# Kernel optimization log

Measured on AMD Instinct MI355X. Metric: run time of the kernel, lower is better.

The kernel has to match this reference:

```python
import jax, jax.numpy as jnp
import numpy as np

B, S, E = 4, 2048, 1024
H, D, F = 16, 64, 4096
EPS = 1e-5


def layer_norm(x, gamma, beta):
    mu = jnp.mean(x, axis=-1, keepdims=True)
    var = jnp.mean(jnp.square(x - mu), axis=-1, keepdims=True)
    return (x - mu) * jax.lax.rsqrt(var + EPS) * gamma + beta


def setup_inputs() -> dict:
    key = jax.random.key(0)
    ks = jax.random.split(key, 8)
    scale = 0.02  # keep logits in a numerically sane range
    X = jax.random.normal(ks[0], (B, S, E), dtype=jnp.float32)
    WQ = jax.random.normal(ks[1], (H, E, D), dtype=jnp.float32) * scale
    WK = jax.random.normal(ks[2], (H, E, D), dtype=jnp.float32) * scale
    WV = jax.random.normal(ks[3], (H, E, D), dtype=jnp.float32) * scale
    WO = jax.random.normal(ks[4], (H * D, E), dtype=jnp.float32) * scale
    gamma = jnp.ones((E,), dtype=jnp.float32)
    beta = jnp.zeros((E,), dtype=jnp.float32)
    W1 = jax.random.normal(ks[5], (E, F), dtype=jnp.float32) * scale
    b1 = jnp.zeros((F,), dtype=jnp.float32)
    W2 = jax.random.normal(ks[6], (F, E), dtype=jnp.float32) * scale
    b2 = jnp.zeros((E,), dtype=jnp.float32)
    return {"X": X, "WQ": WQ, "WK": WK, "WV": WV, "WO": WO,
            "gamma": gamma, "beta": beta, "W1": W1, "b1": b1, "W2": W2, "b2": b2}


def reference(X, WQ, WK, WV, WO, gamma, beta, W1, b1, W2, b2):
    # Batched-over-heads version of the per-head python loop (same math).
    Q = jnp.einsum('bse,hed->bhsd', X, WQ)  # [B,H,S,D]
    K = jnp.einsum('bse,hed->bhsd', X, WK)
    V = jnp.einsum('bse,hed->bhsd', X, WV)
    scores = jnp.einsum('bhsd,bhtd->bhst', Q, K)  # [B,H,S,T]
    # FAITHFUL quirk: torch.softmax(..., dim=1) on a [B,S,S] tensor normalizes
    # over the QUERY axis (axis=2 here), then divides by sqrt(D) AFTER softmax.
    att = jax.nn.softmax(scores, axis=2) / jnp.sqrt(jnp.float32(D))
    vec = jnp.einsum('bhst,bhtd->bhsd', att, V)  # [B,H,S,D]
    att_vec = jnp.transpose(vec, (0, 2, 1, 3)).reshape(X.shape[0], X.shape[1], H * D)
    vector_att = layer_norm(att_vec @ WO + X, gamma, beta)
    vector_ffn = jax.nn.relu(vector_att @ W1 + b1) @ W2 + b2
    return layer_norm(vector_ffn + vector_att, gamma, beta)
```

## Files before the change

kernel.cpp:

```cpp
#include <hip/hip_runtime.h>
#include <cstddef>
#include <cstdint>

#define BB 4
#define SS 2048
#define EE 1024
#define HH 16
#define DD 64
#define FF 4096

typedef unsigned short u16;
typedef __attribute__((ext_vector_type(8))) short short8;
typedef __attribute__((ext_vector_type(4))) short short4v;
typedef __attribute__((ext_vector_type(4))) float f32x4;
typedef __attribute__((ext_vector_type(16))) float f32x16;
typedef __attribute__((ext_vector_type(4))) unsigned u32x4;

__device__ __forceinline__ u16 f2bf(float x) {
    unsigned u = __builtin_bit_cast(unsigned, x);
    u += 0x7fffu + ((u >> 16) & 1u);
    return (u16)(u >> 16);
}
__device__ __forceinline__ float bf2f(u16 h) {
    unsigned u = ((unsigned)h) << 16;
    return __builtin_bit_cast(float, u);
}
__device__ __forceinline__ float ex2(float x) {
    float r;
    asm("v_exp_f32 %0, %1" : "=v"(r) : "v"(x));
    return r;
}
__device__ __forceinline__ unsigned cvtpk(float lo, float hi) {
    unsigned r;
    asm("v_cvt_pk_bf16_f32 %0, %1, %2" : "=v"(r) : "v"(lo), "v"(hi));
    return r;
}
__device__ __forceinline__ void pl32swap(unsigned &a, unsigned &b) {
    asm("s_nop 1\n\tv_permlane32_swap_b32 %0, %1\n\ts_nop 1" : "+v"(a), "+v"(b));
}
__device__ __forceinline__ int sw(int row, int lbyte) {
    return row * 128 + (lbyte ^ ((row & 7) << 4));
}

#define GLD_LDS16(g, l)                                                     \
    __builtin_amdgcn_global_load_lds(                                       \
        (const __attribute__((address_space(1))) void*)(g),                 \
        (__attribute__((address_space(3))) void*)(l), 16, 0, 0)

__global__ __launch_bounds__(256) void cvt_bf(const float* __restrict__ in,
                                              u16* __restrict__ out, int n4) {
    const int i = blockIdx.x * 256 + threadIdx.x;
    if (i < n4) {
        float4 v = reinterpret_cast<const float4*>(in)[i];
        short4v o;
        o.x = (short)f2bf(v.x); o.y = (short)f2bf(v.y);
        o.z = (short)f2bf(v.z); o.w = (short)f2bf(v.w);
        reinterpret_cast<short4v*>(out)[i] = o;
    }
}

__global__ __launch_bounds__(256) void transp_bf(const float* __restrict__ in,
                                                 u16* __restrict__ out, int R, int C) {
    __shared__ float T[64][65];
    const int r0 = blockIdx.x * 64, c0 = blockIdx.y * 64;
    const size_t zoff = (size_t)blockIdx.z * R * C;
    in += zoff; out += zoff;
    const int tid = threadIdx.x;
#pragma unroll 4
    for (int i = 0; i < 16; ++i) {
        int l = tid + i * 256;
        T[l >> 6][l & 63] = in[(size_t)(r0 + (l >> 6)) * C + c0 + (l & 63)];
    }
    __syncthreads();
#pragma unroll 4
    for (int i = 0; i < 16; ++i) {
        int l = tid + i * 256;
        out[(size_t)(c0 + (l >> 6)) * R + r0 + (l & 63)] = f2bf(T[l & 63][l >> 6]);
    }
}

#define WAITV6 asm volatile("s_waitcnt vmcnt(6)" ::: "memory")
#define WAITV0 asm volatile("s_waitcnt vmcnt(0)" ::: "memory")

#define STAGE(p, k0u)                                                         \
    do {                                                                      \
        _Pragma("unroll")                                                     \
        for (int i_ = 0; i_ < 4; ++i_)                                        \
            GLD_LDS16(Ag + (size_t)(i_ * 64) * K + (k0u),                     \
                      &lds[(p) * 24576 + (i_ * 64 + w * 8) * 64]);            \
        _Pragma("unroll")                                                     \
        for (int j_ = 0; j_ < 2; ++j_)                                        \
            GLD_LDS16(Bg + (size_t)(j_ * 64) * K + (k0u),                     \
                      &lds[(p) * 24576 + 16384 + (j_ * 64 + w * 8) * 64]);    \
    } while (0)

template <int EPI>
__global__ __launch_bounds__(512, 2) void gemm256(const u16* __restrict__ A,
                                                  const u16* __restrict__ BT,
                                                  int K, int N, int gy,
                                                  void* __restrict__ Cout,
                                                  const float* __restrict__ bias,
                                                  const void* __restrict__ resid,
                                                  float oscale) {
    __shared__ __align__(16) u16 lds[2 * 24576];
    const int nwg = gridDim.x;
    const int bid = blockIdx.x;
    const int qq = nwg >> 3, rr = nwg & 7;
    const int xcd = bid & 7, lin = bid >> 3;
    const int wgid = (xcd < rr ? xcd * (qq + 1) : rr * (qq + 1) + (xcd - rr) * qq) + lin;
    const int x = wgid / gy, y = wgid % gy;
    const int m0 = x * 256, n0 = y * 128;

    const int tid = threadIdx.x;
    const int w = tid >> 6, l = tid & 63;
    const int l32 = l & 31, hf = l >> 5;
    const int wm = w >> 1, wn = w & 1;

    const int swz = ((l & 7) ^ (l >> 3)) * 8;
    const u16* Ag = A + (size_t)(m0 + w * 8 + (l >> 3)) * K + swz;
    const u16* Bg = BT + (size_t)(n0 + w * 8 + (l >> 3)) * K + swz;

    const int NTt = K >> 6;
    f32x16 acc[2][2] = {};

    STAGE(0, 0);
    STAGE(1, 64);

    for (int t = 0; t < NTt; ++t) {
        const int p = t & 1;
        if (t < NTt - 1) { WAITV6; } else { WAITV0; }
        __builtin_amdgcn_sched_barrier(0);
        __builtin_amdgcn_s_barrier();
        __builtin_amdgcn_sched_barrier(0);
        __builtin_amdgcn_s_setprio(1);
        const u16* Ab = &lds[p * 24576];
        const u16* Bb = &lds[p * 24576 + 16384];
#pragma unroll
        for (int kt = 0; kt < 4; ++kt) {
            const int cs = (((kt * 2 + hf) ^ (l32 & 7)) * 8);
            short8 af[2], bfr[2];
#pragma unroll
            for (int mb = 0; mb < 2; ++mb)
                af[mb] = *(const short8*)&Ab[(wm * 64 + mb * 32 + l32) * 64 + cs];
#pragma unroll
            for (int nb = 0; nb < 2; ++nb)
                bfr[nb] = *(const short8*)&Bb[(wn * 64 + nb * 32 + l32) * 64 + cs];
#pragma unroll
            for (int mb = 0; mb < 2; ++mb)
#pragma unroll
                for (int nb = 0; nb < 2; ++nb)
                    acc[mb][nb] = __builtin_amdgcn_mfma_f32_32x32x16_bf16(af[mb], bfr[nb], acc[mb][nb], 0, 0, 0);
        }
        __builtin_amdgcn_s_setprio(0);
        __builtin_amdgcn_sched_barrier(0);
        __builtin_amdgcn_s_barrier();
        __builtin_amdgcn_sched_barrier(0);
        if (t + 2 < NTt) STAGE(p, (t + 2) * 64);
    }

#pragma unroll
    for (int mb = 0; mb < 2; ++mb)
#pragma unroll
        for (int nb = 0; nb < 2; ++nb) {
            const int col = n0 + wn * 64 + nb * 32 + l32;
#pragma unroll
            for (int r = 0; r < 16; ++r) {
                const int row = m0 + wm * 64 + mb * 32 + (r & 3) + 8 * (r >> 2) + 4 * hf;
                float v = acc[mb][nb][r];
                const size_t idx = (size_t)row * N + col;
                if (EPI == 0) {
                    ((u16*)Cout)[idx] = f2bf(v * oscale);
                } else if (EPI == 1) {
                    ((float*)Cout)[idx] = v + ((const float*)resid)[idx];
                } else if (EPI == 2) {
                    v += bias[col];
                    ((u16*)Cout)[idx] = f2bf(fmaxf(v, 0.f));
                } else {
                    v += bias[col] + bf2f(((const u16*)resid)[idx]);
                    ((float*)Cout)[idx] = v;
                }
            }
        }
}

__global__ __launch_bounds__(256) void stats_l(const u16* __restrict__ Qg,
                                               const u16* __restrict__ Kg,
                                               float* __restrict__ Ls) {
    __shared__ u16 Qt[64 * 72];
    const int t0 = blockIdx.x * 128;
    const int bh = blockIdx.y;
    const int b = bh >> 4, h = bh & 15;
    const int tid = threadIdx.x;
    const int w = tid >> 6, l = tid & 63;
    const int quad = l >> 4, lane16 = l & 15;
    const u16* Qp = Qg + (size_t)b * SS * 1024 + h * 64;
    const u16* Kp = Kg + (size_t)b * SS * 1024 + h * 64;
    const int sr = tid >> 3;
    const int dg = (tid & 7) * 8;

    short8 kf[2][2];
#pragma unroll
    for (int nf = 0; nf < 2; ++nf)
#pragma unroll
        for (int ks = 0; ks < 2; ++ks)
            kf[nf][ks] = *(const short8*)(Kp +
                (size_t)(t0 + w * 32 + nf * 16 + lane16) * 1024 + ks * 32 + quad * 8);

    const u16* qsrc0 = Qp + (size_t)sr * 1024 + dg;
    short8 pq0 = *(const short8*)qsrc0;
    short8 pq1 = *(const short8*)(qsrc0 + (size_t)32 * 1024);

    float lcol[2] = {0.f, 0.f};
    for (int st = 0; st < 32; ++st) {
        __syncthreads();
        *(short8*)&Qt[sr * 72 + dg] = pq0;
        *(short8*)&Qt[(sr + 32) * 72 + dg] = pq1;
        __syncthreads();
        if (st + 1 < 32) {
            const u16* qsrc = Qp + (size_t)((st + 1) * 64 + sr) * 1024 + dg;
            pq0 = *(const short8*)qsrc;
            pq1 = *(const short8*)(qsrc + (size_t)32 * 1024);
        }
        f32x4 sc[4][2] = {};
#pragma unroll
        for (int ks = 0; ks < 2; ++ks) {
#pragma unroll
            for (int mf = 0; mf < 4; ++mf) {
                short8 afr = *(const short8*)&Qt[(mf * 16 + lane16) * 72 + ks * 32 + quad * 8];
#pragma unroll
                for (int nf = 0; nf < 2; ++nf)
                    sc[mf][nf] = __builtin_amdgcn_mfma_f32_16x16x32_bf16(afr, kf[nf][ks], sc[mf][nf], 0, 0, 0);
            }
        }
#pragma unroll
        for (int nf = 0; nf < 2; ++nf)
#pragma unroll
            for (int mf = 0; mf < 4; ++mf)
#pragma unroll
                for (int r = 0; r < 4; ++r) lcol[nf] += ex2(sc[mf][nf][r]);
    }
#pragma unroll
    for (int nf = 0; nf < 2; ++nf) {
        lcol[nf] += __shfl_xor(lcol[nf], 32);
        lcol[nf] += __shfl_xor(lcol[nf], 16);
        if (quad == 0)
            Ls[(size_t)bh * SS + t0 + w * 32 + nf * 16 + lane16] = lcol[nf];
    }
}

__global__ __launch_bounds__(256) void vscale(u16* __restrict__ Vtg,
                                              const float* __restrict__ Ls) {
    const int r = blockIdx.x;
    const int b = blockIdx.y;
    const int h = r >> 6;
    const int t0 = threadIdx.x * 8;
    u16* vp = Vtg + (size_t)r * 8192 + b * SS + t0;
    const float* lp = Ls + (size_t)(b * 16 + h) * SS + t0;
    short8 v = *(short8*)vp;
    short8 o;
#pragma unroll
    for (int i = 0; i < 8; ++i)
        o[i] = (short)f2bf(bf2f((u16)v[i]) * (0.125f / lp[i]));
    *(short8*)vp = o;
}

__global__ __launch_bounds__(256) void pv_fused(const u16* __restrict__ Qg,
                                                const u16* __restrict__ Kg,
                                                const u16* __restrict__ Vtg,
                                                u16* __restrict__ vecbf) {
    __shared__ u16 Ks[64 * 64];
    __shared__ u16 Vs[64 * 64];
    const int s0 = blockIdx.x * 128;
    const int bh = blockIdx.y;
    const int b = bh >> 4, h = bh & 15;
    const int tid = threadIdx.x;
    const int w = tid >> 6, l = tid & 63;
    const int l32 = l & 31, hf = l >> 5;
    const u16* Qp = Qg + (size_t)b * SS * 1024 + h * 64;
    const u16* Kp = Kg + (size_t)b * SS * 1024 + h * 64;
    const u16* Vp = Vtg + (size_t)h * 64 * 8192 + (size_t)b * SS;
    const int sr = tid >> 3, dg = (tid & 7) * 8;

    short8 qf[4];
#pragma unroll
    for (int ks = 0; ks < 4; ++ks)
        qf[ks] = *(const short8*)(Qp + (size_t)(s0 + w * 32 + l32) * 1024 + ks * 16 + hf * 8);

    short8 pk0 = *(const short8*)(Kp + (size_t)sr * 1024 + dg);
    short8 pk1 = *(const short8*)(Kp + (size_t)(sr + 32) * 1024 + dg);
    short8 pv0 = *(const short8*)(Vp + (size_t)sr * 8192 + dg);
    short8 pv1 = *(const short8*)(Vp + (size_t)(sr + 32) * 8192 + dg);

    f32x16 acc[2] = {};
    for (int tt = 0; tt < 32; ++tt) {
        __syncthreads();
        *(short8*)((char*)Ks + sw(sr, dg * 2)) = pk0;
        *(short8*)((char*)Ks + sw(sr + 32, dg * 2)) = pk1;
        *(short8*)((char*)Vs + sw(sr, dg * 2)) = pv0;
        *(short8*)((char*)Vs + sw(sr + 32, dg * 2)) = pv1;
        __syncthreads();
        if (tt + 1 < 32) {
            const int t1 = (tt + 1) * 64;
            pk0 = *(const short8*)(Kp + (size_t)(t1 + sr) * 1024 + dg);
            pk1 = *(const short8*)(Kp + (size_t)(t1 + sr + 32) * 1024 + dg);
            pv0 = *(const short8*)(Vp + (size_t)sr * 8192 + t1 + dg);
            pv1 = *(const short8*)(Vp + (size_t)(sr + 32) * 8192 + t1 + dg);
        }
        f32x16 sc0 = {}, sc1 = {};
#pragma unroll
        for (int ks = 0; ks < 4; ++ks) {
            short8 a0 = *(const short8*)((char*)Ks + sw(l32, ks * 32 + hf * 16));
            short8 a1 = *(const short8*)((char*)Ks + sw(32 + l32, ks * 32 + hf * 16));
            sc0 = __builtin_amdgcn_mfma_f32_32x32x16_bf16(a0, qf[ks], sc0, 0, 0, 0);
            sc1 = __builtin_amdgcn_mfma_f32_32x32x16_bf16(a1, qf[ks], sc1, 0, 0, 0);
        }
        unsigned cp0[8], cp1[8];
#pragma unroll
        for (int p = 0; p < 8; ++p) {
            cp0[p] = cvtpk(ex2(sc0[2 * p]), ex2(sc0[2 * p + 1]));
            cp1[p] = cvtpk(ex2(sc1[2 * p]), ex2(sc1[2 * p + 1]));
        }
        short8 pa[4];
#pragma unroll
        for (int ks2 = 0; ks2 < 4; ++ks2) {
            unsigned* cp = (ks2 & 2) ? cp1 : cp0;
            const int c = (ks2 & 1) * 4;
            unsigned w0 = cp[c + 0], w2 = cp[c + 2];
            unsigned w1 = cp[c + 1], w3 = cp[c + 3];
            pl32swap(w0, w2);
            pl32swap(w1, w3);
            u32x4 t4; t4.x = w0; t4.y = w1; t4.z = w2; t4.w = w3;
            pa[ks2] = __builtin_bit_cast(short8, t4);
        }
#pragma unroll
        for (int ks2 = 0; ks2 < 4; ++ks2)
#pragma unroll
            for (int nf = 0; nf < 2; ++nf) {
                short8 bfr = *(const short8*)((char*)Vs + sw(nf * 32 + l32, ks2 * 32 + hf * 16));
                acc[nf] = __builtin_amdgcn_mfma_f32_32x32x16_bf16(pa[ks2], bfr, acc[nf], 0, 0, 0);
            }
    }
#pragma unroll
    for (int nf = 0; nf < 2; ++nf) {
        const int col = h * 64 + nf * 32 + l32;
#pragma unroll
        for (int r = 0; r < 16; ++r) {
            const int srow = s0 + w * 32 + (r & 3) + 8 * (r >> 2) + 4 * hf;
            vecbf[(size_t)(b * SS + srow) * 1024 + col] = f2bf(acc[nf][r]);
        }
    }
}

__global__ __launch_bounds__(256) void ln_bf_kernel(const float* __restrict__ buf,
                                                    const float* __restrict__ g,
                                                    const float* __restrict__ be,
                                                    u16* __restrict__ outbf) {
    const int row = blockIdx.x;
    const int tid = threadIdx.x;
    const float* p = buf + (size_t)row * EE;
    float4 x = reinterpret_cast<const float4*>(p)[tid];
    float s = x.x + x.y + x.z + x.w;
    __shared__ float red[4];
#pragma unroll
    for (int o = 32; o > 0; o >>= 1) s += __shfl_down(s, o);
    const int wid = tid >> 6, lane = tid & 63;
    if (lane == 0) red[wid] = s;
    __syncthreads();
    const float mu = (red[0] + red[1] + red[2] + red[3]) * (1.0f / EE);
    __syncthreads();
    const float dx = x.x - mu, dy = x.y - mu, dz = x.z - mu, dw = x.w - mu;
    float v = dx * dx + dy * dy + dz * dz + dw * dw;
#pragma unroll
    for (int o = 32; o > 0; o >>= 1) v += __shfl_down(v, o);
    if (lane == 0) red[wid] = v;
    __syncthreads();
    const float var = (red[0] + red[1] + red[2] + red[3]) * (1.0f / EE);
    const float rs = rsqrtf(var + 1e-5f);
    float4 gv = reinterpret_cast<const float4*>(g)[tid];
    float4 bv = reinterpret_cast<const float4*>(be)[tid];
    short4v o;
    o.x = (short)f2bf(dx * rs * gv.x + bv.x);
    o.y = (short)f2bf(dy * rs * gv.y + bv.y);
    o.z = (short)f2bf(dz * rs * gv.z + bv.z);
    o.w = (short)f2bf(dw * rs * gv.w + bv.w);
    reinterpret_cast<short4v*>(outbf + (size_t)row * EE)[tid] = o;
}

__global__ __launch_bounds__(256) void ln_kernel(float* __restrict__ buf,
                                                 const float* __restrict__ g,
                                                 const float* __restrict__ be) {
    const int row = blockIdx.x;
    const int tid = threadIdx.x;
    float* p = buf + (size_t)row * EE;
    float4 x = reinterpret_cast<float4*>(p)[tid];
    float s = x.x + x.y + x.z + x.w;
    __shared__ float red[4];
#pragma unroll
    for (int o = 32; o > 0; o >>= 1) s += __shfl_down(s, o);
    const int wid = tid >> 6, lane = tid & 63;
    if (lane == 0) red[wid] = s;
    __syncthreads();
    const float mu = (red[0] + red[1] + red[2] + red[3]) * (1.0f / EE);
    __syncthreads();
    const float dx = x.x - mu, dy = x.y - mu, dz = x.z - mu, dw = x.w - mu;
    float v = dx * dx + dy * dy + dz * dz + dw * dw;
#pragma unroll
    for (int o = 32; o > 0; o >>= 1) v += __shfl_down(v, o);
    if (lane == 0) red[wid] = v;
    __syncthreads();
    const float var = (red[0] + red[1] + red[2] + red[3]) * (1.0f / EE);
    const float rs = rsqrtf(var + 1e-5f);
    float4 gv = reinterpret_cast<const float4*>(g)[tid];
    float4 bv = reinterpret_cast<const float4*>(be)[tid];
    float4 y;
    y.x = dx * rs * gv.x + bv.x;
    y.y = dy * rs * gv.y + bv.y;
    y.z = dz * rs * gv.z + bv.z;
    y.w = dw * rs * gv.w + bv.w;
    reinterpret_cast<float4*>(p)[tid] = y;
}

extern "C" void kernel_launch(void* const* d_in, const int* in_sizes, int n_in,
                              void* d_out, int out_size, void* d_ws, size_t ws_size,
                              hipStream_t stream) {
    const float* X     = (const float*)d_in[0];
    const float* WQ    = (const float*)d_in[1];
    const float* WK    = (const float*)d_in[2];
    const float* WV    = (const float*)d_in[3];
    const float* WO    = (const float*)d_in[4];
    const float* gamma = (const float*)d_in[5];
    const float* beta  = (const float*)d_in[6];
    const float* W1    = (const float*)d_in[7];
    const float* b1    = (const float*)d_in[8];
    const float* W2    = (const float*)d_in[9];
    const float* b2    = (const float*)d_in[10];
    float* out = (float*)d_out;

    char* ws = (char*)d_ws;
    const size_t MB = 1024 * 1024;
    u16* WQT   = (u16*)(ws + 0);
    u16* WKT   = (u16*)(ws + 2 * MB);
    u16* WVT   = (u16*)(ws + 4 * MB);
    u16* WOT   = (u16*)(ws + 6 * MB);
    u16* W1T   = (u16*)(ws + 8 * MB);
    u16* W2T   = (u16*)(ws + 16 * MB);
    float* Ls  = (float*)(ws + 24 * MB);
    u16* Qbf   = (u16*)(ws + 25 * MB);
    u16* Kbf   = (u16*)(ws + 41 * MB);
    u16* Vt    = (u16*)(ws + 57 * MB);
    u16* vecbf = (u16*)(ws + 73 * MB);
    u16* hid   = (u16*)(ws + 25 * MB);
    u16* Xbf   = (u16*)(ws + 89 * MB);
    float* vatt  = (float*)(ws + 105 * MB);
    u16*   ln1bf = (u16*)(ws + 137 * MB);

    const int NT = BB * SS;

    cvt_bf<<<8192, 256, 0, stream>>>(X, Xbf, NT * EE / 4);
    transp_bf<<<dim3(16, 1, 16), 256, 0, stream>>>(WQ, WQT, EE, DD);
    transp_bf<<<dim3(16, 1, 16), 256, 0, stream>>>(WK, WKT, EE, DD);
    transp_bf<<<dim3(16, 1, 16), 256, 0, stream>>>(WV, WVT, EE, DD);
    transp_bf<<<dim3(16, 16, 1), 256, 0, stream>>>(WO, WOT, HH * DD, EE);
    transp_bf<<<dim3(16, 64, 1), 256, 0, stream>>>(W1, W1T, EE, FF);
    transp_bf<<<dim3(64, 16, 1), 256, 0, stream>>>(W2, W2T, FF, EE);

    gemm256<0><<<256, 512, 0, stream>>>(Xbf, WQT, 1024, 1024, 8, Qbf, nullptr, nullptr, 1.44269504089f);
    gemm256<0><<<256, 512, 0, stream>>>(Xbf, WKT, 1024, 1024, 8, Kbf, nullptr, nullptr, 1.0f);
    gemm256<0><<<256, 512, 0, stream>>>(WVT, Xbf, 1024, 8192, 64, Vt, nullptr, nullptr, 1.0f);

    stats_l<<<dim3(SS / 128, BB * HH), 256, 0, stream>>>(Qbf, Kbf, Ls);
    vscale<<<dim3(1024, BB), 256, 0, stream>>>(Vt, Ls);
    pv_fused<<<dim3(SS / 128, BB * HH), 256, 0, stream>>>(Qbf, Kbf, Vt, vecbf);

    gemm256<1><<<256, 512, 0, stream>>>(vecbf, WOT, 1024, 1024, 8, vatt, nullptr, X, 1.0f);
    ln_bf_kernel<<<NT, 256, 0, stream>>>(vatt, gamma, beta, ln1bf);

    gemm256<2><<<1024, 512, 0, stream>>>(ln1bf, W1T, 1024, FF, 32, hid, b1, nullptr, 1.0f);
    gemm256<3><<<256, 512, 0, stream>>>(hid, W2T, FF, 1024, 8, out, b2, ln1bf, 1.0f);

    ln_kernel<<<NT, 256, 0, stream>>>(out, gamma, beta);
}
```

Baseline: 586.5 us.

## Fuse V scaling into stats kernel and double-buffer attention LDS tiles

```diff
diff --git a/kernel.cpp b/kernel.cpp
--- a/kernel.cpp
+++ b/kernel.cpp
@@ -12,7 +12,6 @@
 typedef unsigned short u16;
 typedef __attribute__((ext_vector_type(8))) short short8;
 typedef __attribute__((ext_vector_type(4))) short short4v;
-typedef __attribute__((ext_vector_type(4))) float f32x4;
 typedef __attribute__((ext_vector_type(16))) float f32x16;
 typedef __attribute__((ext_vector_type(4))) unsigned u32x4;
 
@@ -35,8 +34,13 @@
     asm("v_cvt_pk_bf16_f32 %0, %1, %2" : "=v"(r) : "v"(lo), "v"(hi));
     return r;
 }
-__device__ __forceinline__ void pl32swap(unsigned &a, unsigned &b) {
-    asm("s_nop 1\n\tv_permlane32_swap_b32 %0, %1\n\ts_nop 1" : "+v"(a), "+v"(b));
+__device__ __forceinline__ void pl32swap2(unsigned &a, unsigned &b,
+                                          unsigned &c, unsigned &d) {
+    asm("s_nop 1\n\t"
+        "v_permlane32_swap_b32 %0, %1\n\t"
+        "v_permlane32_swap_b32 %2, %3\n\t"
+        "s_nop 1"
+        : "+v"(a), "+v"(b), "+v"(c), "+v"(d));
 }
 __device__ __forceinline__ int sw(int row, int lbyte) {
     return row * 128 + (lbyte ^ ((row & 7) << 4));
@@ -183,95 +187,90 @@
         }
 }
 
-__global__ __launch_bounds__(256) void stats_l(const u16* __restrict__ Qg,
+__global__ __launch_bounds__(256) void stats32(const u16* __restrict__ Qg,
                                                const u16* __restrict__ Kg,
-                                               float* __restrict__ Ls) {
-    __shared__ u16 Qt[64 * 72];
-    const int t0 = blockIdx.x * 128;
-    const int bh = blockIdx.y;
+                                               u16* __restrict__ Vtg) {
+    __shared__ u16 Qs[2][64 * 64];
+    __shared__ float lbuf[128];
+    const int bid = blockIdx.x;
+    const int wgid = (bid & 7) * 128 + (bid >> 3);
+    const int t0 = (wgid & 15) * 128;
+    const int bh = wgid >> 4;
     const int b = bh >> 4, h = bh & 15;
     const int tid = threadIdx.x;
     const int w = tid >> 6, l = tid & 63;
-    const int quad = l >> 4, lane16 = l & 15;
+    const int l32 = l & 31, hf = l >> 5;
     const u16* Qp = Qg + (size_t)b * SS * 1024 + h * 64;
     const u16* Kp = Kg + (size_t)b * SS * 1024 + h * 64;
-    const int sr = tid >> 3;
-    const int dg = (tid & 7) * 8;
-
-    short8 kf[2][2];
-#pragma unroll
-    for (int nf = 0; nf < 2; ++nf)
-#pragma unroll
-        for (int ks = 0; ks < 2; ++ks)
-            kf[nf][ks] = *(const short8*)(Kp +
-                (size_t)(t0 + w * 32 + nf * 16 + lane16) * 1024 + ks * 32 + quad * 8);
-
-    const u16* qsrc0 = Qp + (size_t)sr * 1024 + dg;
-    short8 pq0 = *(const short8*)qsrc0;
-    short8 pq1 = *(const short8*)(qsrc0 + (size_t)32 * 1024);
-
-    float lcol[2] = {0.f, 0.f};
+    const int sr = tid >> 3, dg = (tid & 7) * 8;
+
+    short8 kf[4];
+#pragma unroll
+    for (int ks = 0; ks < 4; ++ks)
+        kf[ks] = *(const short8*)(Kp + (size_t)(t0 + w * 32 + l32) * 1024 + ks * 16 + hf * 8);
+
+    short8 pq0 = *(const short8*)(Qp + (size_t)sr * 1024 + dg);
+    short8 pq1 = *(const short8*)(Qp + (size_t)(sr + 32) * 1024 + dg);
+    *(short8*)((char*)Qs[0] + sw(sr, dg * 2)) = pq0;
+    *(short8*)((char*)Qs[0] + sw(sr + 32, dg * 2)) = pq1;
+    pq0 = *(const short8*)(Qp + (size_t)(64 + sr) * 1024 + dg);
+    pq1 = *(const short8*)(Qp + (size_t)(64 + sr + 32) * 1024 + dg);
+    __syncthreads();
+
+    float ls0 = 0.f, ls1 = 0.f;
     for (int st = 0; st < 32; ++st) {
+        const int p = st & 1;
+        if (st + 1 < 32) {
+            *(short8*)((char*)Qs[p ^ 1] + sw(sr, dg * 2)) = pq0;
+            *(short8*)((char*)Qs[p ^ 1] + sw(sr + 32, dg * 2)) = pq1;
+        }
+        if (st + 2 < 32) {
+            const int s1 = (st + 2) * 64;
+            pq0 = *(const short8*)(Qp + (size_t)(s1 + sr) * 1024 + dg);
+            pq1 = *(const short8*)(Qp + (size_t)(s1 + sr + 32) * 1024 + dg);
+        }
+        f32x16 sc0 = {}, sc1 = {};
+        __builtin_amdgcn_s_setprio(1);
+#pragma unroll
+        for (int ks = 0; ks < 4; ++ks) {
+            short8 a0 = *(const short8*)((char*)Qs[p] + sw(l32, ks * 32 + hf * 16));
+            short8 a1 = *(const short8*)((char*)Qs[p] + sw(32 + l32, ks * 32 + hf * 16));
+            sc0 = __builtin_amdgcn_mfma_f32_32x32x16_bf16(a0, kf[ks], sc0, 0, 0, 0);
+            sc1 = __builtin_amdgcn_mfma_f32_32x32x16_bf16(a1, kf[ks], sc1, 0, 0, 0);
+        }
+        __builtin_amdgcn_s_setprio(0);
+#pragma unroll
+        for (int r = 0; r < 16; ++r) { ls0 += ex2(sc0[r]); ls1 += ex2(sc1[r]); }
         __syncthreads();
-        *(short8*)&Qt[sr * 72 + dg] = pq0;
-        *(short8*)&Qt[(sr + 32) * 72 + dg] = pq1;
-        __syncthreads();
-        if (st + 1 < 32) {
-            const u16* qsrc = Qp + (size_t)((st + 1) * 64 + sr) * 1024 + dg;
-            pq0 = *(const short8*)qsrc;
-            pq1 = *(const short8*)(qsrc + (size_t)32 * 1024);
-        }
-        f32x4 sc[4][2] = {};
-#pragma unroll
-        for (int ks = 0; ks < 2; ++ks) {
-#pragma unroll
-            for (int mf = 0; mf < 4; ++mf) {
-                short8 afr = *(const short8*)&Qt[(mf * 16 + lane16) * 72 + ks * 32 + quad * 8];
-#pragma unroll
-                for (int nf = 0; nf < 2; ++nf)
-                    sc[mf][nf] = __builtin_amdgcn_mfma_f32_16x16x32_bf16(afr, kf[nf][ks], sc[mf][nf], 0, 0, 0);
-            }
-        }
-#pragma unroll
-        for (int nf = 0; nf < 2; ++nf)
-#pragma unroll
-            for (int mf = 0; mf < 4; ++mf)
-#pragma unroll
-                for (int r = 0; r < 4; ++r) lcol[nf] += ex2(sc[mf][nf][r]);
-    }
-#pragma unroll
-    for (int nf = 0; nf < 2; ++nf) {
-        lcol[nf] += __shfl_xor(lcol[nf], 32);
-        lcol[nf] += __shfl_xor(lcol[nf], 16);
-        if (quad == 0)
-            Ls[(size_t)bh * SS + t0 + w * 32 + nf * 16 + lane16] = lcol[nf];
-    }
-}
-
-__global__ __launch_bounds__(256) void vscale(u16* __restrict__ Vtg,
-                                              const float* __restrict__ Ls) {
-    const int r = blockIdx.x;
-    const int b = blockIdx.y;
-    const int h = r >> 6;
-    const int t0 = threadIdx.x * 8;
-    u16* vp = Vtg + (size_t)r * 8192 + b * SS + t0;
-    const float* lp = Ls + (size_t)(b * 16 + h) * SS + t0;
-    short8 v = *(short8*)vp;
-    short8 o;
-#pragma unroll
-    for (int i = 0; i < 8; ++i)
-        o[i] = (short)f2bf(bf2f((u16)v[i]) * (0.125f / lp[i]));
-    *(short8*)vp = o;
+    }
+    float lsum = ls0 + ls1;
+    lsum += __shfl_xor(lsum, 32);
+    if (hf == 0) lbuf[w * 32 + l32] = 0.125f / lsum;
+    __syncthreads();
+
+    const int d = tid >> 2, cb = (tid & 3) * 32;
+    u16* vp = Vtg + (size_t)(h * 64 + d) * 8192 + b * SS + t0 + cb;
+#pragma unroll
+    for (int j = 0; j < 4; ++j) {
+        short8 v = *(short8*)(vp + j * 8);
+        short8 o;
+#pragma unroll
+        for (int i = 0; i < 8; ++i)
+            o[i] = (short)f2bf(bf2f((u16)v[i]) * lbuf[cb + j * 8 + i]);
+        *(short8*)(vp + j * 8) = o;
+    }
 }
 
 __global__ __launch_bounds__(256) void pv_fused(const u16* __restrict__ Qg,
                                                 const u16* __restrict__ Kg,
                                                 const u16* __restrict__ Vtg,
                                                 u16* __restrict__ vecbf) {
-    __shared__ u16 Ks[64 * 64];
-    __shared__ u16 Vs[64 * 64];
-    const int s0 = blockIdx.x * 128;
-    const int bh = blockIdx.y;
+    __shared__ u16 Ks[2][64 * 64];
+    __shared__ u16 Vs[2][64 * 64];
+    const int bid = blockIdx.x;
+    const int wgid = (bid & 7) * 128 + (bid >> 3);
+    const int s0 = (wgid & 15) * 128;
+    const int bh = wgid >> 4;
     const int b = bh >> 4, h = bh & 15;
     const int tid = threadIdx.x;
     const int w = tid >> 6, l = tid & 63;
@@ -290,35 +289,47 @@
     short8 pk1 = *(const short8*)(Kp + (size_t)(sr + 32) * 1024 + dg);
     short8 pv0 = *(const short8*)(Vp + (size_t)sr * 8192 + dg);
     short8 pv1 = *(const short8*)(Vp + (size_t)(sr + 32) * 8192 + dg);
+    *(short8*)((char*)Ks[0] + sw(sr, dg * 2)) = pk0;
+    *(short8*)((char*)Ks[0] + sw(sr + 32, dg * 2)) = pk1;
+    *(short8*)((char*)Vs[0] + sw(sr, dg * 2)) = pv0;
+    *(short8*)((char*)Vs[0] + sw(sr + 32, dg * 2)) = pv1;
+    pk0 = *(const short8*)(Kp + (size_t)(64 + sr) * 1024 + dg);
+    pk1 = *(const short8*)(Kp + (size_t)(64 + sr + 32) * 1024 + dg);
+    pv0 = *(const short8*)(Vp + (size_t)sr * 8192 + 64 + dg);
+    pv1 = *(const short8*)(Vp + (size_t)(sr + 32) * 8192 + 64 + dg);
+    __syncthreads();
 
     f32x16 acc[2] = {};
     for (int tt = 0; tt < 32; ++tt) {
-        __syncthreads();
-        *(short8*)((char*)Ks + sw(sr, dg * 2)) = pk0;
-        *(short8*)((char*)Ks + sw(sr + 32, dg * 2)) = pk1;
-        *(short8*)((char*)Vs + sw(sr, dg * 2)) = pv0;
-        *(short8*)((char*)Vs + sw(sr + 32, dg * 2)) = pv1;
-        __syncthreads();
+        const int p = tt & 1;
         if (tt + 1 < 32) {
-            const int t1 = (tt + 1) * 64;
+            *(short8*)((char*)Ks[p ^ 1] + sw(sr, dg * 2)) = pk0;
+            *(short8*)((char*)Ks[p ^ 1] + sw(sr + 32, dg * 2)) = pk1;
+            *(short8*)((char*)Vs[p ^ 1] + sw(sr, dg * 2)) = pv0;
+            *(short8*)((char*)Vs[p ^ 1] + sw(sr + 32, dg * 2)) = pv1;
+        }
+        if (tt + 2 < 32) {
+            const int t1 = (tt + 2) * 64;
             pk0 = *(const short8*)(Kp + (size_t)(t1 + sr) * 1024 + dg);
             pk1 = *(const short8*)(Kp + (size_t)(t1 + sr + 32) * 1024 + dg);
             pv0 = *(const short8*)(Vp + (size_t)sr * 8192 + t1 + dg);
             pv1 = *(const short8*)(Vp + (size_t)(sr + 32) * 8192 + t1 + dg);
         }
         f32x16 sc0 = {}, sc1 = {};
+        __builtin_amdgcn_s_setprio(1);
 #pragma unroll
         for (int ks = 0; ks < 4; ++ks) {
-            short8 a0 = *(const short8*)((char*)Ks + sw(l32, ks * 32 + hf * 16));
-            short8 a1 = *(const short8*)((char*)Ks + sw(32 + l32, ks * 32 + hf * 16));
+            short8 a0 = *(const short8*)((char*)Ks[p] + sw(l32, ks * 32 + hf * 16));
+            short8 a1 = *(const short8*)((char*)Ks[p] + sw(32 + l32, ks * 32 + hf * 16));
             sc0 = __builtin_amdgcn_mfma_f32_32x32x16_bf16(a0, qf[ks], sc0, 0, 0, 0);
             sc1 = __builtin_amdgcn_mfma_f32_32x32x16_bf16(a1, qf[ks], sc1, 0, 0, 0);
         }
+        __builtin_amdgcn_s_setprio(0);
         unsigned cp0[8], cp1[8];
 #pragma unroll
-        for (int p = 0; p < 8; ++p) {
-            cp0[p] = cvtpk(ex2(sc0[2 * p]), ex2(sc0[2 * p + 1]));
-            cp1[p] = cvtpk(ex2(sc1[2 * p]), ex2(sc1[2 * p + 1]));
+        for (int p2 = 0; p2 < 8; ++p2) {
+            cp0[p2] = cvtpk(ex2(sc0[2 * p2]), ex2(sc0[2 * p2 + 1]));
+            cp1[p2] = cvtpk(ex2(sc1[2 * p2]), ex2(sc1[2 * p2 + 1]));
         }
         short8 pa[4];
 #pragma unroll
@@ -327,18 +338,20 @@
             const int c = (ks2 & 1) * 4;
             unsigned w0 = cp[c + 0], w2 = cp[c + 2];
             unsigned w1 = cp[c + 1], w3 = cp[c + 3];
-            pl32swap(w0, w2);
-            pl32swap(w1, w3);
+            pl32swap2(w0, w2, w1, w3);
             u32x4 t4; t4.x = w0; t4.y = w1; t4.z = w2; t4.w = w3;
             pa[ks2] = __builtin_bit_cast(short8, t4);
         }
+        __builtin_amdgcn_s_setprio(1);
 #pragma unroll
         for (int ks2 = 0; ks2 < 4; ++ks2)
 #pragma unroll
             for (int nf = 0; nf < 2; ++nf) {
-                short8 bfr = *(const short8*)((char*)Vs + sw(nf * 32 + l32, ks2 * 32 + hf * 16));
+                short8 bfr = *(const short8*)((char*)Vs[p] + sw(nf * 32 + l32, ks2 * 32 + hf * 16));
                 acc[nf] = __builtin_amdgcn_mfma_f32_32x32x16_bf16(pa[ks2], bfr, acc[nf], 0, 0, 0);
             }
+        __builtin_amdgcn_s_setprio(0);
+        __syncthreads();
     }
 #pragma unroll
     for (int nf = 0; nf < 2; ++nf) {
@@ -444,7 +457,6 @@
     u16* WOT   = (u16*)(ws + 6 * MB);
     u16* W1T   = (u16*)(ws + 8 * MB);
     u16* W2T   = (u16*)(ws + 16 * MB);
-    float* Ls  = (float*)(ws + 24 * MB);
     u16* Qbf   = (u16*)(ws + 25 * MB);
     u16* Kbf   = (u16*)(ws + 41 * MB);
     u16* Vt    = (u16*)(ws + 57 * MB);
@@ -468,9 +480,8 @@
     gemm256<0><<<256, 512, 0, stream>>>(Xbf, WKT, 1024, 1024, 8, Kbf, nullptr, nullptr, 1.0f);
     gemm256<0><<<256, 512, 0, stream>>>(WVT, Xbf, 1024, 8192, 64, Vt, nullptr, nullptr, 1.0f);
 
-    stats_l<<<dim3(SS / 128, BB * HH), 256, 0, stream>>>(Qbf, Kbf, Ls);
-    vscale<<<dim3(1024, BB), 256, 0, stream>>>(Vt, Ls);
-    pv_fused<<<dim3(SS / 128, BB * HH), 256, 0, stream>>>(Qbf, Kbf, Vt, vecbf);
+    stats32<<<1024, 256, 0, stream>>>(Qbf, Kbf, Vt);
+    pv_fused<<<1024, 256, 0, stream>>>(Qbf, Kbf, Vt, vecbf);
 
     gemm256<1><<<256, 512, 0, stream>>>(vecbf, WOT, 1024, 1024, 8, vatt, nullptr, X, 1.0f);
     ln_bf_kernel<<<NT, 256, 0, stream>>>(vatt, gamma, beta, ln1bf);
```

Result: faster. 574.8 us (-2.0%).
